# Kernel tuning notes

Hardware: AMD Instinct MI355X
Metric: run time of the kernel (lower is better)

## Reference

```python
import jax, jax.numpy as jnp
import numpy as np

B, T, D_MODEL = 2, 2048, 2048
D_HEAD = 128
H_PER_G = 4
N_GROUPS = D_MODEL // (H_PER_G * D_HEAD)  # 4
ROT_BASE = 10000
EPS = 1e-6


def setup_inputs() -> dict:
    key = jax.random.key(0)
    ks = jax.random.split(key, 5)
    s = D_MODEL ** -0.5
    return {
        "x": jax.random.normal(ks[0], (B, T, D_MODEL), jnp.float32),
        "wq": jax.random.normal(ks[1], (D_MODEL, D_MODEL), jnp.float32) * s,
        "wk": jax.random.normal(ks[2], (D_MODEL, D_MODEL // H_PER_G), jnp.float32) * s,
        "wv": jax.random.normal(ks[3], (D_MODEL, D_MODEL // H_PER_G), jnp.float32) * s,
        "wo": jax.random.normal(ks[4], (D_MODEL, D_MODEL), jnp.float32) * s,
        "gq": jnp.ones((N_GROUPS, H_PER_G, D_HEAD), jnp.float32),
        "gk": jnp.ones((N_GROUPS, D_HEAD), jnp.float32),
    }


def _rmsnorm(t):
    rms = jnp.sqrt(jnp.mean(jnp.square(t), axis=-1, keepdims=True) + EPS)
    return t / rms


def _rope(t):
    # t: [..., length, width]
    length, width = t.shape[-2], t.shape[-1]
    pos = jnp.arange(length)[:, None]                       # [t,1]
    dims = jnp.arange(width // 2)[None, :]                  # [1,d/2]
    ang = jnp.power(float(ROT_BASE), -dims / (width // 2))
    rad = (pos * ang).astype(t.dtype)                       # [t,d/2]
    cos, sin = jnp.cos(rad), jnp.sin(rad)
    even, odd = jnp.split(t, 2, axis=-1)
    return jnp.concatenate([even * cos - odd * sin, even * sin + odd * cos], axis=-1)


def reference(x, wq, wk, wv, wo, gq, gk):
    b, t, _ = x.shape
    q = jnp.einsum('bti,io->bto', x, wq)
    k = jnp.einsum('bti,io->bto', x, wk)
    v = jnp.einsum('bti,io->bto', x, wv)
    # b t (g h d) -> b g h t d ; b t (g d) -> b g t d
    q = q.reshape(b, t, N_GROUPS, H_PER_G, D_HEAD).transpose(0, 2, 3, 1, 4)
    k = k.reshape(b, t, N_GROUPS, D_HEAD).transpose(0, 2, 1, 3)
    v = v.reshape(b, t, N_GROUPS, D_HEAD).transpose(0, 2, 1, 3)
    # QK RMSNorm with gains
    q = _rmsnorm(q) * gq[None, :, :, None, :]
    k = _rmsnorm(k) * gk[None, :, None, :]
    # RoPE
    q = _rope(q)
    k = _rope(k)
    mult = jnp.asarray(D_HEAD ** -0.25, x.dtype)
    s = jnp.einsum('bghid,bgjd->bghij', q * mult, k * mult)
    # causal mask: subtract 1e30 where i < j
    i = jnp.arange(t)[:, None]
    j = jnp.arange(t)[None, :]
    s = s - jnp.asarray(1e30, s.dtype) * (i < j)
    p = jax.nn.softmax(s, axis=-1)
    o = jnp.einsum('bghij,bgjd->bghid', p, v)
    o = o.transpose(0, 3, 1, 2, 4).reshape(b, t, D_MODEL)
    return jnp.einsum('bti,io->bto', o, wo)
```

## Files before the change

### kernel.cpp

```cpp
#include <hip/hip_runtime.h>
#include <cstdint>

typedef unsigned short u16;
typedef __attribute__((ext_vector_type(8))) __bf16 bf16x8;
typedef __attribute__((ext_vector_type(4))) float f32x4;
typedef __attribute__((ext_vector_type(16))) float f32x16;
typedef __attribute__((ext_vector_type(8))) unsigned short u16x8;

#define DEV __device__ __forceinline__

DEV u16 f2bf(float f) {
  __bf16 b = (__bf16)f;
  return __builtin_bit_cast(u16, b);
}
DEV float bf2f(u16 h) { return __uint_as_float(((unsigned)h) << 16); }
DEV float exp2_fast(float x) { float r; asm("v_exp_f32 %0, %1" : "=v"(r) : "v"(x)); return r; }
DEV void barrier_mem() { asm volatile("s_barrier" ::: "memory"); }

typedef __attribute__((address_space(1))) void gvoid_t;
typedef __attribute__((address_space(3))) void lvoid_t;

DEV void gload_lds16(const void* g, void* l) {
  __builtin_amdgcn_global_load_lds((gvoid_t*)(void*)(uintptr_t)g,
                                   (lvoid_t*)l, 16, 0, 0);
}

#define B_   2
#define T_   2048
#define DM   2048
#define MROWS (B_*T_)
#define QSC  0.1275174f

__global__ void k_prep(const float* __restrict__ x,
                       const float* __restrict__ wq, const float* __restrict__ wk,
                       const float* __restrict__ wv, const float* __restrict__ wo,
                       u16* __restrict__ xb, u16* __restrict__ wqkvt,
                       u16* __restrict__ wot, float2* __restrict__ rope) {
  const int bid = blockIdx.x;
  const int tid = threadIdx.x;
  if (bid < 8192) {
    int i = bid * 256 + tid;
    float4 v = ((const float4*)x)[i];
    ((ushort4*)xb)[i] = make_ushort4(f2bf(v.x), f2bf(v.y), f2bf(v.z), f2bf(v.w));
    return;
  }
  if (bid >= 18432) {
    int i = (bid - 18432) * 256 + tid;
    int pos = i >> 6, d = i & 63;
    float ang = powf(10000.0f, -(float)d / 64.0f);
    float s, c;
    sincosf((float)pos * ang, &s, &c);
    rope[i] = make_float2(c, s);
    return;
  }
  __shared__ float tile[32][33];
  const int tb = bid - 8192;
  const float* in;
  u16* out;
  int C, bx, by, crow0;
  if (tb < 4096)      { in = wq; out = wqkvt; C = 2048; bx = tb & 63;          by = tb >> 6;          crow0 = 0; }
  else if (tb < 5120) { in = wk; out = wqkvt; C = 512;  bx = (tb - 4096) & 15; by = (tb - 4096) >> 4; crow0 = 2048; }
  else if (tb < 6144) { in = wv; out = wqkvt; C = 512;  bx = (tb - 5120) & 15; by = (tb - 5120) >> 4; crow0 = 2560; }
  else                { in = wo; out = wot;   C = 2048; bx = (tb - 6144) & 63; by = (tb - 6144) >> 6; crow0 = 0; }
  const int c0 = bx * 32, r0 = by * 32;
  const int tx = tid & 31, ty = tid >> 5;
  #pragma unroll
  for (int j = 0; j < 32; j += 8)
    tile[ty + j][tx] = in[(size_t)(r0 + ty + j) * C + c0 + tx];
  __syncthreads();
  #pragma unroll
  for (int j = 0; j < 32; j += 8)
    out[(size_t)(crow0 + c0 + ty + j) * 2048 + r0 + tx] = f2bf(tile[tx][ty + j]);
}

template <typename OutT>
__global__ __launch_bounds__(256) void k_gemm(
    const u16* __restrict__ A, const u16* __restrict__ BT, OutT* __restrict__ C,
    int M, int N, int K) {
  __shared__ u16 As[128 * 64];
  __shared__ u16 Bs[128 * 64];
  const int tid = threadIdx.x;
  const int w = tid >> 6, lane = tid & 63;
  const int lr32 = lane & 31, l5 = lane >> 5;
  const int nx = gridDim.x;
  const int flat = blockIdx.y * nx + blockIdx.x;
  const int cpx = (nx * gridDim.y) >> 3;
  const int f = (flat & 7) * cpx + (flat >> 3);
  const int m0 = (f / nx) * 128, n0 = (f % nx) * 128;
  const int wr = w >> 1, wc = w & 1;
  f32x16 acc[2][2] = {};
  for (int k0 = 0; k0 < K; k0 += 64) {
    __syncthreads();
    #pragma unroll
    for (int i = 0; i < 4; i++) {
      int idx = i * 256 + tid;
      int row = idx >> 3, blk = idx & 7;
      int scol = ((blk ^ (row & 7)) << 3);
      gload_lds16(&A[(size_t)(m0 + row) * K + k0 + scol], &As[(idx & ~63) * 8]);
      gload_lds16(&BT[(size_t)(n0 + row) * K + k0 + scol], &Bs[(idx & ~63) * 8]);
    }
    __syncthreads();
    #pragma unroll
    for (int kc = 0; kc < 4; kc++) {
      bf16x8 af[2], bfr[2];
      #pragma unroll
      for (int m = 0; m < 2; m++) {
        int row = wr * 64 + m * 32 + lr32;
        int blk = (kc * 2 + l5) ^ (row & 7);
        af[m] = *(const bf16x8*)&As[row * 64 + (blk << 3)];
      }
      #pragma unroll
      for (int n = 0; n < 2; n++) {
        int row = wc * 64 + n * 32 + lr32;
        int blk = (kc * 2 + l5) ^ (row & 7);
        bfr[n] = *(const bf16x8*)&Bs[row * 64 + (blk << 3)];
      }
      #pragma unroll
      for (int m = 0; m < 2; m++)
        #pragma unroll
        for (int n = 0; n < 2; n++)
          acc[m][n] = __builtin_amdgcn_mfma_f32_32x32x16_bf16(af[m], bfr[n], acc[m][n], 0, 0, 0);
    }
  }
  #pragma unroll
  for (int m = 0; m < 2; m++)
    #pragma unroll
    for (int n = 0; n < 2; n++)
      #pragma unroll
      for (int reg = 0; reg < 16; reg++) {
        int row = m0 + wr * 64 + m * 32 + (reg & 3) + 8 * (reg >> 2) + 4 * l5;
        int col = n0 + wc * 64 + n * 32 + lr32;
        if constexpr (sizeof(OutT) == 2) C[(size_t)row * N + col] = f2bf(acc[m][n][reg]);
        else                             C[(size_t)row * N + col] = acc[m][n][reg];
      }
}

__global__ void k_postgemm(const u16* __restrict__ qkvf, const float* __restrict__ gk,
                           const float2* __restrict__ tab, u16* __restrict__ kb,
                           u16* __restrict__ vt) {
  const int bid = blockIdx.x;
  const int w = threadIdx.x >> 6, lane = threadIdx.x & 63;
  if (bid < 4096) {
    int W = bid * 4 + w;
    int g = W & 3;
    int bt = W >> 2;
    int t = bt & 2047, b = bt >> 11;
    const u16* row = qkvf + (size_t)bt * 3072 + 2048 + (size_t)g * 128;
    float v0 = bf2f(row[lane]);
    float v1 = bf2f(row[lane + 64]);
    float ss = v0 * v0 + v1 * v1;
    #pragma unroll
    for (int off = 1; off < 64; off <<= 1) ss += __shfl_xor(ss, off, 64);
    float inv = 1.0f / sqrtf(ss * (1.0f / 128.0f) + 1e-6f);
    v0 *= inv * gk[g * 128 + lane];
    v1 *= inv * gk[g * 128 + 64 + lane];
    float2 cs = tab[t * 64 + lane];
    float o0 = v0 * cs.x - v1 * cs.y;
    float o1 = v0 * cs.y + v1 * cs.x;
    u16* orow = kb + ((size_t)((b * 4 + g) * 2048 + t)) * 128;
    orow[lane] = f2bf(o0);
    orow[lane + 64] = f2bf(o1);
  } else {
    int W = (bid - 4096) * 4 + w;
    int t8 = W & 255, dh = (W >> 8) & 1, bg = W >> 9;
    int b = bg >> 2, g = bg & 3;
    int t0 = t8 * 8;
    int d = dh * 64 + lane;
    u16x8 pack;
    #pragma unroll
    for (int j = 0; j < 8; j++)
      pack[j] = qkvf[(size_t)(b * 2048 + t0 + j) * 3072 + 2560 + g * 128 + d];
    *(u16x8*)&vt[((size_t)(bg * 128 + d)) * 2048 + t0] = pack;
  }
}

DEV void stage_tiles(const u16* kh, const u16* vh, int j0, u16* Kbuf, u16* Vbuf, int tid) {
  #pragma unroll
  for (int i = 0; i < 4; i++) {
    int idx = i * 256 + tid;
    int row = idx >> 4, blk = idx & 15;
    gload_lds16(&kh[(size_t)(j0 + row) * 128 + ((blk ^ (row & 7)) << 3)],
                &Kbuf[(idx & ~63) * 8]);
  }
  #pragma unroll
  for (int i = 0; i < 4; i++) {
    int idx = i * 256 + tid;
    int row = idx >> 3, blk = idx & 7;
    gload_lds16(&vh[(size_t)row * T_ + j0 + ((blk ^ (row & 7)) << 3)],
                &Vbuf[(idx & ~63) * 8]);
  }
}

DEV void attn_tile(const u16* __restrict__ Kc, const u16* __restrict__ Vc,
                   u16* __restrict__ Psw, const bf16x8* qf, f32x4* oacc,
                   float& lsum, int lr, int lg, int w, bool diag) {
  f32x4 s[4] = {};
  __builtin_amdgcn_s_setprio(1);
  #pragma unroll
  for (int kk = 0; kk < 4; kk++) {
    #pragma unroll
    for (int c = 0; c < 4; c++) {
      const int kvr = c * 16 + lr;
      bf16x8 kf = *(const bf16x8*)&Kc[kvr * 128 + (((kk * 4 + lg) ^ (kvr & 7)) << 3)];
      s[c] = __builtin_amdgcn_mfma_f32_16x16x32_bf16(kf, qf[kk], s[c], 0, 0, 0);
    }
  }
  __builtin_amdgcn_s_setprio(0);
  if (diag) {
    #pragma unroll
    for (int c = 0; c < 4; c++)
      #pragma unroll
      for (int r = 0; r < 4; r++)
        if (c * 16 + lg * 4 + r > w * 16 + lr) s[c][r] = -1.0e30f;
  }
  float rs = 0.f;
  #pragma unroll
  for (int c = 0; c < 4; c++)
    #pragma unroll
    for (int r = 0; r < 4; r++) {
      float pv = exp2_fast(s[c][r]);
      s[c][r] = pv;
      rs += pv;
    }
  lsum += rs;
  #pragma unroll
  for (int c = 0; c < 4; c++) {
    ushort4 q4 = make_ushort4(f2bf(s[c][0]), f2bf(s[c][1]), f2bf(s[c][2]), f2bf(s[c][3]));
    int blk8 = (c * 4 + lg) ^ ((lr & 7) << 1);
    *(ushort4*)&Psw[lr * 64 + blk8 * 4] = q4;
  }
  #pragma unroll
  for (int ks = 0; ks < 2; ks++) {
    bf16x8 pf = *(const bf16x8*)&Psw[lr * 64 +
                 (((2 * (ks * 4 + lg)) ^ ((lr & 7) << 1)) << 2)];
    __builtin_amdgcn_s_setprio(1);
    #pragma unroll
    for (int nd = 0; nd < 8; nd++) {
      const int d = nd * 16 + lr;
      bf16x8 vf = *(const bf16x8*)&Vc[d * 64 + (((ks * 4 + lg) ^ (d & 7)) << 3)];
      oacc[nd] = __builtin_amdgcn_mfma_f32_16x16x32_bf16(pf, vf, oacc[nd], 0, 0, 0);
    }
    __builtin_amdgcn_s_setprio(0);
  }
}

DEV void attn_epilogue(u16* __restrict__ ob, int b, int g, int h, int q0,
                       const f32x4* oacc, float lsum, int lr, int lg, int w) {
  lsum += __shfl_xor(lsum, 16, 64);
  lsum += __shfl_xor(lsum, 32, 64);
  float inv = 1.0f / lsum;
  float iv[4];
  #pragma unroll
  for (int r = 0; r < 4; r++) iv[r] = __shfl(inv, lg * 4 + r, 64);
  #pragma unroll
  for (int r = 0; r < 4; r++) {
    int orow = q0 + w * 16 + lg * 4 + r;
    size_t base = (size_t)(b * T_ + orow) * 2048 + (size_t)(g * 4 + h) * 128;
    #pragma unroll
    for (int nd = 0; nd < 8; nd++)
      ob[base + nd * 16 + lr] = f2bf(oacc[nd][r] * iv[r]);
  }
}

__global__ __launch_bounds__(256) void k_attn(
    const u16* __restrict__ qkvf, const float* __restrict__ gq,
    const float2* __restrict__ rope, const u16* __restrict__ kb,
    const u16* __restrict__ vtb, u16* __restrict__ ob) {
  __shared__ __align__(16) u16 Ks[2][64 * 128];
  __shared__ __align__(16) u16 Vs[2][128 * 64];
  __shared__ __align__(16) u16 Ps[4][16 * 64];
  const int bid = blockIdx.x;
  const int hg = bid & 7;
  const int rest = bid >> 3;
  const int hh = rest & 3;
  const int p = rest >> 2;
  const int b = hg >> 2, g = hg & 3, h = hh;
  const int tid = threadIdx.x;
  const int w = tid >> 6, lane = tid & 63;
  const int lr = lane & 15, lg = lane >> 4;
  const u16* kh = kb + (size_t)hg * (T_ * 128);
  const u16* vh = vtb + (size_t)hg * (128 * T_);
  const float* gqh = gq + (size_t)(g * 4 + h) * 128;

  #pragma unroll 1
  for (int half = 0; half < 2; ++half) {
    const int qblk = half ? p : 31 - p;
    const int q0 = qblk * 64;
    bf16x8 qf[4];
    {
      const int qrow = q0 + w * 16 + lr;
      const u16* qsrc = qkvf + (size_t)(b * T_ + qrow) * 3072 + (size_t)(g * 4 + h) * 128;
      float qe[4][8];
      float ss = 0.f;
      #pragma unroll
      for (int kk = 0; kk < 4; kk++) {
        u16x8 raw = *(const u16x8*)&qsrc[kk * 32 + lg * 8];
        #pragma unroll
        for (int j = 0; j < 8; j++) {
          float v = bf2f(raw[j]);
          qe[kk][j] = v;
          ss += v * v;
        }
      }
      ss += __shfl_xor(ss, 16, 64);
      ss += __shfl_xor(ss, 32, 64);
      float inv = 1.0f / sqrtf(ss * (1.0f / 128.0f) + 1e-6f);
      #pragma unroll
      for (int kk = 0; kk < 2; kk++) {
        const float2* tp = &rope[(size_t)qrow * 64 + kk * 32 + lg * 8];
        u16x8 lo, hi;
        #pragma unroll
        for (int j = 0; j < 8; j++) {
          int d = kk * 32 + lg * 8 + j;
          float v0 = qe[kk][j] * inv * gqh[d];
          float v1 = qe[kk + 2][j] * inv * gqh[d + 64];
          float2 cs = tp[j];
          lo[j] = f2bf((v0 * cs.x - v1 * cs.y) * QSC);
          hi[j] = f2bf((v0 * cs.y + v1 * cs.x) * QSC);
        }
        qf[kk] = __builtin_bit_cast(bf16x8, lo);
        qf[kk + 2] = __builtin_bit_cast(bf16x8, hi);
      }
    }

    f32x4 oacc[8] = {};
    float lsum = 0.f;

    stage_tiles(kh, vh, 0, Ks[0], Vs[0], tid);
    asm volatile("s_waitcnt vmcnt(0)" ::: "memory");
    barrier_mem();
    int cur = 0;
    for (int jt = 0; jt <= qblk; ++jt) {
      if (jt < qblk)
        stage_tiles(kh, vh, (jt + 1) * 64, Ks[cur ^ 1], Vs[cur ^ 1], tid);
      attn_tile(Ks[cur], Vs[cur], Ps[w], qf, oacc, lsum, lr, lg, w, jt == qblk);
      asm volatile("s_waitcnt vmcnt(0)" ::: "memory");
      barrier_mem();
      cur ^= 1;
    }
    attn_epilogue(ob, b, g, h, q0, oacc, lsum, lr, lg, w);
  }
}

#define OFF_XB    ((size_t)0)
#define OFF_WQKVT ((size_t)16777216)
#define OFF_WOT   ((size_t)29360128)
#define OFF_ROPE  ((size_t)37748736)
#define OFF_OB    ((size_t)38797312)
#define OFF_KB    ((size_t)55574528)
#define OFF_VTB   ((size_t)59768832)
#define OFF_QKVF  ((size_t)63963136)

extern "C" void kernel_launch(void* const* d_in, const int* in_sizes, int n_in,
                              void* d_out, int out_size, void* d_ws, size_t ws_size,
                              hipStream_t stream) {
  const float* x  = (const float*)d_in[0];
  const float* wq = (const float*)d_in[1];
  const float* wk = (const float*)d_in[2];
  const float* wv = (const float*)d_in[3];
  const float* wo = (const float*)d_in[4];
  const float* gq = (const float*)d_in[5];
  const float* gk = (const float*)d_in[6];
  float* out = (float*)d_out;
  char* ws = (char*)d_ws;

  u16*    xb    = (u16*)(ws + OFF_XB);
  u16*    wqkvt = (u16*)(ws + OFF_WQKVT);
  u16*    wot   = (u16*)(ws + OFF_WOT);
  float2* rope  = (float2*)(ws + OFF_ROPE);
  u16*    obuf  = (u16*)(ws + OFF_OB);
  u16*    kbuf  = (u16*)(ws + OFF_KB);
  u16*    vtb   = (u16*)(ws + OFF_VTB);
  u16*    qkvf  = (u16*)(ws + OFF_QKVF);

  k_prep<<<18944, 256, 0, stream>>>(x, wq, wk, wv, wo, xb, wqkvt, wot, rope);
  k_gemm<u16><<<dim3(24, 32), 256, 0, stream>>>(xb, wqkvt, qkvf, MROWS, 3072, 2048);
  k_postgemm<<<5120, 256, 0, stream>>>(qkvf, gk, rope, kbuf, vtb);
  k_attn<<<512, 256, 0, stream>>>(qkvf, gq, rope, kbuf, vtb, obuf);
  k_gemm<float><<<dim3(16, 32), 256, 0, stream>>>(obuf, wot, out, MROWS, 2048, 2048);
}
```

Baseline: 192.3 us.

## Split attention tile work 2x2 across query and key halves per wave

Each wave now handles 32 query rows against half of the 64-key tile, instead of 16 query rows against the full tile. Each K fragment and V fragment loaded from LDS now feeds two MFMAs, which halves LDS fragment reads per MFMA. The two key-half partial outputs and row sums are combined through LDS at the end, reusing the K buffer and adding extra barriers. Register pressure rises because each wave holds two accumulator sets.

New measurement: 239.0 us. 1.24x slower.

```diff
diff --git a/kernel.cpp b/kernel.cpp
--- a/kernel.cpp
+++ b/kernel.cpp
@@ -191,84 +191,14 @@
   }
 }
 
-DEV void attn_tile(const u16* __restrict__ Kc, const u16* __restrict__ Vc,
-                   u16* __restrict__ Psw, const bf16x8* qf, f32x4* oacc,
-                   float& lsum, int lr, int lg, int w, bool diag) {
-  f32x4 s[4] = {};
-  __builtin_amdgcn_s_setprio(1);
-  #pragma unroll
-  for (int kk = 0; kk < 4; kk++) {
-    #pragma unroll
-    for (int c = 0; c < 4; c++) {
-      const int kvr = c * 16 + lr;
-      bf16x8 kf = *(const bf16x8*)&Kc[kvr * 128 + (((kk * 4 + lg) ^ (kvr & 7)) << 3)];
-      s[c] = __builtin_amdgcn_mfma_f32_16x16x32_bf16(kf, qf[kk], s[c], 0, 0, 0);
-    }
-  }
-  __builtin_amdgcn_s_setprio(0);
-  if (diag) {
-    #pragma unroll
-    for (int c = 0; c < 4; c++)
-      #pragma unroll
-      for (int r = 0; r < 4; r++)
-        if (c * 16 + lg * 4 + r > w * 16 + lr) s[c][r] = -1.0e30f;
-  }
-  float rs = 0.f;
-  #pragma unroll
-  for (int c = 0; c < 4; c++)
-    #pragma unroll
-    for (int r = 0; r < 4; r++) {
-      float pv = exp2_fast(s[c][r]);
-      s[c][r] = pv;
-      rs += pv;
-    }
-  lsum += rs;
-  #pragma unroll
-  for (int c = 0; c < 4; c++) {
-    ushort4 q4 = make_ushort4(f2bf(s[c][0]), f2bf(s[c][1]), f2bf(s[c][2]), f2bf(s[c][3]));
-    int blk8 = (c * 4 + lg) ^ ((lr & 7) << 1);
-    *(ushort4*)&Psw[lr * 64 + blk8 * 4] = q4;
-  }
-  #pragma unroll
-  for (int ks = 0; ks < 2; ks++) {
-    bf16x8 pf = *(const bf16x8*)&Psw[lr * 64 +
-                 (((2 * (ks * 4 + lg)) ^ ((lr & 7) << 1)) << 2)];
-    __builtin_amdgcn_s_setprio(1);
-    #pragma unroll
-    for (int nd = 0; nd < 8; nd++) {
-      const int d = nd * 16 + lr;
-      bf16x8 vf = *(const bf16x8*)&Vc[d * 64 + (((ks * 4 + lg) ^ (d & 7)) << 3)];
-      oacc[nd] = __builtin_amdgcn_mfma_f32_16x16x32_bf16(pf, vf, oacc[nd], 0, 0, 0);
-    }
-    __builtin_amdgcn_s_setprio(0);
-  }
-}
-
-DEV void attn_epilogue(u16* __restrict__ ob, int b, int g, int h, int q0,
-                       const f32x4* oacc, float lsum, int lr, int lg, int w) {
-  lsum += __shfl_xor(lsum, 16, 64);
-  lsum += __shfl_xor(lsum, 32, 64);
-  float inv = 1.0f / lsum;
-  float iv[4];
-  #pragma unroll
-  for (int r = 0; r < 4; r++) iv[r] = __shfl(inv, lg * 4 + r, 64);
-  #pragma unroll
-  for (int r = 0; r < 4; r++) {
-    int orow = q0 + w * 16 + lg * 4 + r;
-    size_t base = (size_t)(b * T_ + orow) * 2048 + (size_t)(g * 4 + h) * 128;
-    #pragma unroll
-    for (int nd = 0; nd < 8; nd++)
-      ob[base + nd * 16 + lr] = f2bf(oacc[nd][r] * iv[r]);
-  }
-}
-
 __global__ __launch_bounds__(256) void k_attn(
     const u16* __restrict__ qkvf, const float* __restrict__ gq,
     const float2* __restrict__ rope, const u16* __restrict__ kb,
     const u16* __restrict__ vtb, u16* __restrict__ ob) {
   __shared__ __align__(16) u16 Ks[2][64 * 128];
   __shared__ __align__(16) u16 Vs[2][128 * 64];
-  __shared__ __align__(16) u16 Ps[4][16 * 64];
+  __shared__ __align__(16) u16 Ps[4][2][16 * 40];
+  __shared__ float Lx[2][2][16];
   const int bid = blockIdx.x;
   const int hg = bid & 7;
   const int rest = bid >> 3;
@@ -278,6 +208,7 @@
   const int tid = threadIdx.x;
   const int w = tid >> 6, lane = tid & 63;
   const int lr = lane & 15, lg = lane >> 4;
+  const int qh = w >> 1, kvh = w & 1;
   const u16* kh = kb + (size_t)hg * (T_ * 128);
   const u16* vh = vtb + (size_t)hg * (128 * T_);
   const float* gqh = gq + (size_t)(g * 4 + h) * 128;
@@ -286,9 +217,10 @@
   for (int half = 0; half < 2; ++half) {
     const int qblk = half ? p : 31 - p;
     const int q0 = qblk * 64;
-    bf16x8 qf[4];
-    {
-      const int qrow = q0 + w * 16 + lr;
+    bf16x8 qf[2][4];
+    #pragma unroll
+    for (int t = 0; t < 2; t++) {
+      const int qrow = q0 + qh * 32 + t * 16 + lr;
       const u16* qsrc = qkvf + (size_t)(b * T_ + qrow) * 3072 + (size_t)(g * 4 + h) * 128;
       float qe[4][8];
       float ss = 0.f;
@@ -318,13 +250,13 @@
           lo[j] = f2bf((v0 * cs.x - v1 * cs.y) * QSC);
           hi[j] = f2bf((v0 * cs.y + v1 * cs.x) * QSC);
         }
-        qf[kk] = __builtin_bit_cast(bf16x8, lo);
-        qf[kk + 2] = __builtin_bit_cast(bf16x8, hi);
-      }
-    }
-
-    f32x4 oacc[8] = {};
-    float lsum = 0.f;
+        qf[t][kk] = __builtin_bit_cast(bf16x8, lo);
+        qf[t][kk + 2] = __builtin_bit_cast(bf16x8, hi);
+      }
+    }
+
+    f32x4 oacc[2][8] = {};
+    float lsum[2] = {0.f, 0.f};
 
     stage_tiles(kh, vh, 0, Ks[0], Vs[0], tid);
     asm volatile("s_waitcnt vmcnt(0)" ::: "memory");
@@ -333,12 +265,104 @@
     for (int jt = 0; jt <= qblk; ++jt) {
       if (jt < qblk)
         stage_tiles(kh, vh, (jt + 1) * 64, Ks[cur ^ 1], Vs[cur ^ 1], tid);
-      attn_tile(Ks[cur], Vs[cur], Ps[w], qf, oacc, lsum, lr, lg, w, jt == qblk);
+      const u16* Kc = Ks[cur];
+      const u16* Vc = Vs[cur];
+      f32x4 s[2][2] = {};
+      __builtin_amdgcn_s_setprio(1);
+      #pragma unroll
+      for (int kk = 0; kk < 4; kk++) {
+        #pragma unroll
+        for (int c = 0; c < 2; c++) {
+          const int kvr = kvh * 32 + c * 16 + lr;
+          bf16x8 kf = *(const bf16x8*)&Kc[kvr * 128 + (((kk * 4 + lg) ^ (kvr & 7)) << 3)];
+          s[0][c] = __builtin_amdgcn_mfma_f32_16x16x32_bf16(kf, qf[0][kk], s[0][c], 0, 0, 0);
+          s[1][c] = __builtin_amdgcn_mfma_f32_16x16x32_bf16(kf, qf[1][kk], s[1][c], 0, 0, 0);
+        }
+      }
+      __builtin_amdgcn_s_setprio(0);
+      if (jt == qblk) {
+        #pragma unroll
+        for (int t = 0; t < 2; t++)
+          #pragma unroll
+          for (int c = 0; c < 2; c++)
+            #pragma unroll
+            for (int r = 0; r < 4; r++)
+              if (kvh * 32 + c * 16 + lg * 4 + r > qh * 32 + t * 16 + lr)
+                s[t][c][r] = -1.0e30f;
+      }
+      #pragma unroll
+      for (int t = 0; t < 2; t++) {
+        float rs = 0.f;
+        #pragma unroll
+        for (int c = 0; c < 2; c++)
+          #pragma unroll
+          for (int r = 0; r < 4; r++) {
+            float pv = exp2_fast(s[t][c][r]);
+            s[t][c][r] = pv;
+            rs += pv;
+          }
+        lsum[t] += rs;
+        #pragma unroll
+        for (int c = 0; c < 2; c++) {
+          ushort4 q4 = make_ushort4(f2bf(s[t][c][0]), f2bf(s[t][c][1]),
+                                    f2bf(s[t][c][2]), f2bf(s[t][c][3]));
+          int B16 = (c * 2 + (lg >> 1)) ^ (lr & 3);
+          *(ushort4*)&Ps[w][t][lr * 40 + B16 * 8 + (lg & 1) * 4] = q4;
+        }
+      }
+      bf16x8 pf0 = *(const bf16x8*)&Ps[w][0][lr * 40 + ((lg ^ (lr & 3)) << 3)];
+      bf16x8 pf1 = *(const bf16x8*)&Ps[w][1][lr * 40 + ((lg ^ (lr & 3)) << 3)];
+      __builtin_amdgcn_s_setprio(1);
+      #pragma unroll
+      for (int nd = 0; nd < 8; nd++) {
+        const int dg = nd * 16 + lr;
+        bf16x8 vf = *(const bf16x8*)&Vc[dg * 64 + (((kvh * 4 + lg) ^ (dg & 7)) << 3)];
+        oacc[0][nd] = __builtin_amdgcn_mfma_f32_16x16x32_bf16(pf0, vf, oacc[0][nd], 0, 0, 0);
+        oacc[1][nd] = __builtin_amdgcn_mfma_f32_16x16x32_bf16(pf1, vf, oacc[1][nd], 0, 0, 0);
+      }
+      __builtin_amdgcn_s_setprio(0);
       asm volatile("s_waitcnt vmcnt(0)" ::: "memory");
       barrier_mem();
       cur ^= 1;
     }
-    attn_epilogue(ob, b, g, h, q0, oacc, lsum, lr, lg, w);
+    #pragma unroll
+    for (int t = 0; t < 2; t++) {
+      lsum[t] += __shfl_xor(lsum[t], 16, 64);
+      lsum[t] += __shfl_xor(lsum[t], 32, 64);
+    }
+    __syncthreads();
+    float* ox = (float*)&Ks[0][0];
+    if (kvh == 1) {
+      #pragma unroll
+      for (int t = 0; t < 2; t++) {
+        #pragma unroll
+        for (int nd = 0; nd < 8; nd++)
+          *(f32x4*)&ox[((((qh * 2 + t) * 8) + nd) * 64 + lane) * 4] = oacc[t][nd];
+        if (lg == 0) Lx[qh][t][lr] = lsum[t];
+      }
+    }
+    __syncthreads();
+    if (kvh == 0) {
+      #pragma unroll
+      for (int t = 0; t < 2; t++) {
+        #pragma unroll
+        for (int nd = 0; nd < 8; nd++)
+          oacc[t][nd] += *(const f32x4*)&ox[((((qh * 2 + t) * 8) + nd) * 64 + lane) * 4];
+        float inv = 1.0f / (lsum[t] + Lx[qh][t][lr]);
+        float iv[4];
+        #pragma unroll
+        for (int r = 0; r < 4; r++) iv[r] = __shfl(inv, lg * 4 + r, 64);
+        #pragma unroll
+        for (int r = 0; r < 4; r++) {
+          int orow = q0 + qh * 32 + t * 16 + lg * 4 + r;
+          size_t base = (size_t)(b * T_ + orow) * 2048 + (size_t)(g * 4 + h) * 128;
+          #pragma unroll
+          for (int nd = 0; nd < 8; nd++)
+            ob[base + nd * 16 + lr] = f2bf(oacc[t][nd][r] * iv[r]);
+        }
+      }
+    }
+    __syncthreads();
   }
 }
 
```
